# Performance work log

Measured on AMD Instinct MI355X. Metric: run time of the kernel, lower is better.

## Reference

```python
import jax, jax.numpy as jnp
import numpy as np

B, C, D, L, H = 128, 1000, 300, 40, 100


def setup_inputs() -> dict:
    key = jax.random.key(0)
    ks = jax.random.split(key, 16)
    def rn(i, shape, sc=1.0):
        return (jax.random.normal(ks[i], shape, jnp.float32) * sc).astype(jnp.float32)
    return {
        "utt": rn(0, (B, L, D)),
        "sys_slots": rn(1, (B, D), 0.1),
        "conf_slots": rn(2, (B, D), 0.1),
        "conf_values": rn(3, (B, D), 0.1),
        "y_past_state": jax.random.uniform(ks[4], (B, C), jnp.float32),
        "slot_emb": rn(5, (C, D), 0.1),
        "value_emb": rn(6, (C, D), 0.1),
        "Wc": rn(7, (D, 2 * D), 0.05), "bc": jnp.zeros((D,), jnp.float32),
        "conv_w1": rn(8, (D, D, 1), 0.05), "conv_b1": jnp.zeros((D,), jnp.float32),
        "conv_w2": rn(9, (D, D, 2), 0.05), "conv_b2": jnp.zeros((D,), jnp.float32),
        "conv_w3": rn(10, (D, D, 3), 0.05), "conv_b3": jnp.zeros((D,), jnp.float32),
        "Wd": rn(11, (H, D), 0.05), "bd": jnp.zeros((H,), jnp.float32),
        "Wmr": rn(12, (H, D), 0.05), "bmr": jnp.zeros((H,), jnp.float32),
        "Wmc": rn(13, (H, D), 0.05), "bmc": jnp.zeros((H,), jnp.float32),
        "Wj": rn(14, (1, H), 0.05), "bj": jnp.zeros((1,), jnp.float32),
    }


def _conv_relu_pool(x_ncl, w, b):
    # x_ncl: [B, D, L]; w: [F, D, k] -> relu(conv) then global max-pool over time -> [B, F]
    y = jax.lax.conv_general_dilated(x_ncl, w, (1,), 'VALID',
                                     dimension_numbers=('NCH', 'OIH', 'NCH'))
    y = jax.nn.relu(y + b[None, :, None])
    return jnp.max(y, axis=2)


def _sig_linear(x, W, b):
    # Sequential(Sigmoid, Linear): Linear applied to sigmoid(x)
    return jax.nn.sigmoid(x) @ W.T + b


def reference(utt, sys_slots, conf_slots, conf_values, y_past_state,
              slot_emb, value_emb, Wc, bc,
              conv_w1, conv_b1, conv_w2, conv_b2, conv_w3, conv_b3,
              Wd, bd, Wmr, bmr, Wmc, bmc, Wj, bj):
    # CNN utterance encoder: sum of 3 conv branches (filter widths 1,2,3)
    x = jnp.transpose(utt, (0, 2, 1))  # [B, D, L]
    final_utt = (_conv_relu_pool(x, conv_w1, conv_b1)
                 + _conv_relu_pool(x, conv_w2, conv_b2)
                 + _conv_relu_pool(x, conv_w3, conv_b3))  # [B, D]

    # candidates_transform = sigmoid(Linear(cat(slot_emb, value_emb)))
    cand = jax.nn.sigmoid(jnp.concatenate([slot_emb, value_emb], axis=1) @ Wc.T + bc)  # [C, D]

    # fused version of the per-batch repeat/addcmul loop: [B, C, D]
    contrib = cand[None, :, :] * final_utt[:, None, :]

    y1 = _sig_linear(_sig_linear(contrib, Wd, bd), Wj, bj)  # [B, C, 1]

    # system-act request gate: ([C,D]@[D,B]) @ [B,D] -> [C, D]
    m_r = (slot_emb @ sys_slots.T) @ final_utt
    y2 = _sig_linear(_sig_linear(m_r, Wmr, bmr), Wj, bj)  # [C, 1]

    # system-act confirm gate
    m_c = ((slot_emb @ conf_slots.T) * (value_emb @ conf_values.T)) @ final_utt  # [C, D]
    y3 = _sig_linear(_sig_linear(m_c, Wmc, bmc), Wj, bj)  # [C, 1]

    y_presoftmax = y1 + y2[None, :, :] + y3[None, :, :]  # [B, C, 1]
    combine = 0.5
    return combine * y_presoftmax[..., 0] + (1.0 - combine) * y_past_state  # [B, C]
```

## Files before the change

### kernel.cpp

```cpp
#include <hip/hip_runtime.h>
#include <hip/hip_bf16.h>

#define OFF_Y23     0
#define OFF_BDP     4096
#define OFF_WJP     4544
#define OFF_BCP     4992
#define OFF_BMRP    6272
#define OFF_BMCP    6720
#define OFF_WALLT   7168
#define OFF_FUBF    1235968
#define OFF_FUBFT   1317888
#define OFF_CATSV   1399808
#define OFF_WCPK    2710528
#define OFF_CANDBF  3120128
#define OFF_WDFRAG  3775488
#define OFF_WMRFRAG 3847168
#define OFF_WMCFRAG 3918848
#define OFF_SYSB    3990528
#define OFF_CONFSB  4072448
#define OFF_CONFVB  4154368
#define OFF_PRBF    4236288
#define OFF_PCBF    4498432
#define OFF_SMRBF   4760576
#define OFF_SMCBF   5415936
#define OFF_XBF     6071296

typedef short bf16x8_t __attribute__((ext_vector_type(8)));
typedef float f32x4_t  __attribute__((ext_vector_type(4)));

__device__ __forceinline__ float sigmoidf_fast(float x) {
    return __builtin_amdgcn_rcpf(1.0f + __expf(-x));
}
__device__ __forceinline__ unsigned short f2bf(float x) {
    unsigned int u = __float_as_uint(x);
    unsigned int r = (u + 0x7FFFu + ((u >> 16) & 1u)) >> 16;
    return (unsigned short)r;
}
__device__ __forceinline__ float bf2f(unsigned short h) {
    return __uint_as_float(((unsigned int)h) << 16);
}

__global__ __launch_bounds__(256) void pack_kernel(const float* __restrict__ w1,
        const float* __restrict__ w2, const float* __restrict__ w3,
        const float* __restrict__ Wc, const float* __restrict__ Wd,
        const float* __restrict__ Wmr, const float* __restrict__ Wmc,
        const float* __restrict__ sys, const float* __restrict__ confs,
        const float* __restrict__ confv, const float* __restrict__ bd,
        const float* __restrict__ Wj, const float* __restrict__ bmr,
        const float* __restrict__ bmc, const float* __restrict__ bc,
        const float* __restrict__ slot, const float* __restrict__ value,
        const float* __restrict__ utt,
        unsigned short* __restrict__ WallTbf, unsigned short* __restrict__ WdFrag,
        unsigned short* __restrict__ WmrFrag, unsigned short* __restrict__ WmcFrag,
        float* __restrict__ bdPad, float* __restrict__ WjPad,
        float* __restrict__ bmrPad, float* __restrict__ bmcPad,
        float* __restrict__ bcPad,
        unsigned short* __restrict__ sysB, unsigned short* __restrict__ confsB,
        unsigned short* __restrict__ confvB, unsigned short* __restrict__ catsv,
        unsigned short* __restrict__ WcPk, unsigned short* __restrict__ Xbf) {
    int t = blockIdx.x * 256 + threadIdx.x;
    union { unsigned short u[8]; uint4 q; } o;
    if (t < 76800) {
        int i8 = t * 8;
        int tap = i8 / 102400;
        int rem = i8 - tap * 102400;
        int f = rem / 320, k0 = rem % 320;
        #pragma unroll
        for (int e = 0; e < 8; e++) {
            int k = k0 + e;
            float v = 0.0f;
            if (f < 300 && k < 300) {
                int fd = f * 300 + k;
                v = (tap == 0) ? w1[fd] : (tap == 1) ? w2[fd * 2]
                  : (tap == 2) ? w2[fd * 2 + 1] : w3[fd * 3 + (tap - 3)];
            }
            o.u[e] = f2bf(v);
        }
        *(uint4*)(WallTbf + i8) = o.q;
    } else if (t < 90240) {
        int ent = t - 76800;
        int mat = ent / 4480;
        int le = ent - mat * 4480;
        const float* W = (mat == 0) ? Wd : ((mat == 1) ? Wmr : Wmc);
        unsigned short* dst = (mat == 0) ? WdFrag : ((mat == 1) ? WmrFrag : WmcFrag);
        int kt = le / 448;
        int r = le - kt * 448;
        int ni = r >> 6, lane = r & 63;
        int j = ni * 16 + (lane & 15);
        int kb = kt * 32 + (lane >> 4) * 8;
        #pragma unroll
        for (int e = 0; e < 8; e++) {
            int k = kb + e;
            o.u[e] = f2bf((j < 100 && k < 300) ? W[j * 300 + k] : 0.0f);
        }
        *(uint4*)(dst + le * 8) = o.q;
    } else if (t < 105600) {
        int i8 = (t - 90240) * 8;
        int m = i8 / 40960, r = i8 - m * 40960;
        int bb = r / 320, k0 = r % 320;
        const float* src = (m == 0) ? sys : ((m == 1) ? confs : confv);
        unsigned short* dst = (m == 0) ? sysB : ((m == 1) ? confsB : confvB);
        #pragma unroll
        for (int e = 0; e < 8; e++) {
            int k = k0 + e;
            o.u[e] = f2bf((k < 300) ? src[bb * 300 + k] : 0.0f);
        }
        *(uint4*)(dst + r) = o.q;
    } else if (t < 187520) {
        int i8 = (t - 105600) * 8;
        int c = i8 / 640, k0 = i8 % 640;
        #pragma unroll
        for (int e = 0; e < 8; e++) {
            int k = k0 + e;
            float v = 0.0f;
            if (c < 1000) {
                if (k < 300)                  v = slot[c * 300 + k];
                else if (k >= 320 && k < 620) v = value[c * 300 + (k - 320)];
            }
            o.u[e] = f2bf(v);
        }
        *(uint4*)(catsv + i8) = o.q;
    } else if (t < 213120) {
        int i8 = (t - 187520) * 8;
        int f = i8 / 640, k0 = i8 % 640;
        #pragma unroll
        for (int e = 0; e < 8; e++) {
            int k = k0 + e;
            float v = 0.0f;
            if (f < 300) {
                if (k < 300)                  v = Wc[f * 600 + k];
                else if (k >= 320 && k < 620) v = Wc[f * 600 + 300 + (k - 320)];
            }
            o.u[e] = f2bf(v);
        }
        *(uint4*)(WcPk + i8) = o.q;
    } else if (t < 417920) {
        int i8 = (t - 213120) * 8;
        int m = i8 / 320, k0 = i8 % 320;
        if (k0 + 8 <= 300) {
            float4 a = *(const float4*)(utt + m * 300 + k0);
            float4 b = *(const float4*)(utt + m * 300 + k0 + 4);
            o.u[0] = f2bf(a.x); o.u[1] = f2bf(a.y); o.u[2] = f2bf(a.z); o.u[3] = f2bf(a.w);
            o.u[4] = f2bf(b.x); o.u[5] = f2bf(b.y); o.u[6] = f2bf(b.z); o.u[7] = f2bf(b.w);
        } else {
            #pragma unroll
            for (int e = 0; e < 8; e++) {
                int k = k0 + e;
                o.u[e] = f2bf((k < 300) ? utt[m * 300 + k] : 0.0f);
            }
        }
        *(uint4*)(Xbf + i8) = o.q;
    } else if (t < 418688) {
        int j = t - 417920;
        if (j < 112)      bdPad[j] = (j < 100) ? bd[j] : 0.0f;
        else if (j < 224) { int jj = j - 112; WjPad[jj]  = (jj < 100) ? Wj[jj]  : 0.0f; }
        else if (j < 336) { int jj = j - 224; bmrPad[jj] = (jj < 100) ? bmr[jj] : 0.0f; }
        else if (j < 448) { int jj = j - 336; bmcPad[jj] = (jj < 100) ? bmc[jj] : 0.0f; }
        else              { int jj = j - 448; bcPad[jj]  = (jj < 300) ? bc[jj]  : 0.0f; }
    }
}

__global__ __launch_bounds__(256, 4) void early_kernel(
        const unsigned short* __restrict__ Xbf, const unsigned short* __restrict__ WallTbf,
        const float* __restrict__ b1, const float* __restrict__ b2,
        const float* __restrict__ b3,
        unsigned short* __restrict__ fubf, unsigned short* __restrict__ fubfT,
        const unsigned short* __restrict__ catsv, const unsigned short* __restrict__ WcPk,
        const float* __restrict__ bcPad, unsigned short* __restrict__ candbf,
        const unsigned short* __restrict__ sysB, const unsigned short* __restrict__ confsB,
        const unsigned short* __restrict__ confvB,
        unsigned short* __restrict__ Prbf, unsigned short* __restrict__ Pcbf) {
    __shared__ __attribute__((aligned(16))) char smem[25600];
    const int bid = blockIdx.x;
    const int tid = threadIdx.x;
    const int lane = tid & 63, w = tid >> 6;
    const int ln = lane & 15, lq = lane >> 4;

    if (bid >= 112) {
        short* As = (short*)smem;
        short* Bs = (short*)(smem + 3840);
        short* Ps = (short*)smem;
        const int g = bid - 112;
        const int xcd = g & 7;
        const int idx2 = g >> 3;
        const int b = xcd * 16 + idx2 / 10;
        const int fb = idx2 % 10;
        f32x4_t acc[3][3];
        #pragma unroll
        for (int i = 0; i < 3; i++)
            #pragma unroll
            for (int j = 0; j < 3; j++) acc[i][j] = (f32x4_t){0.f, 0.f, 0.f, 0.f};

        const int arow = tid >> 2, aq = tid & 3;
        int agrow = b * 40 + arow; if (agrow > 5119) agrow = 5119;
        const unsigned short* aSrc = Xbf + agrow * 320 + aq * 8;
        const unsigned short* bSrc[3];
        #pragma unroll
        for (int s = 0; s < 3; s++) {
            int i2 = tid + 256 * s;
            int nr = i2 >> 2, q = i2 & 3;
            int tap = nr >> 5, f = fb * 32 + (nr & 31);
            bSrc[s] = WallTbf + (tap * 320 + f) * 320 + q * 8;
        }
        uint4 pa = {0, 0, 0, 0}, pb[3];
        if (tid < 192) pa = *(const uint4*)aSrc;
        #pragma unroll
        for (int s = 0; s < 3; s++) pb[s] = *(const uint4*)bSrc[s];
        if (tid < 192) *(uint4*)(&As[arow * 40 + aq * 8]) = pa;
        #pragma unroll
        for (int s = 0; s < 3; s++) {
            int i2 = tid + 256 * s;
            int nr = i2 >> 2, q = i2 & 3;
            *(uint4*)(&Bs[nr * 40 + q * 8]) = pb[s];
        }
        __syncthreads();

        #pragma unroll 1
        for (int kt = 0; kt < 10; kt++) {
            if (kt < 9) {
                int kk2 = (kt + 1) * 32;
                if (tid < 192) pa = *(const uint4*)(aSrc + kk2);
                #pragma unroll
                for (int s = 0; s < 3; s++) pb[s] = *(const uint4*)(bSrc[s] + kk2);
            }
            bf16x8_t a[3], bb[3];
            #pragma unroll
            for (int mi = 0; mi < 3; mi++)
                a[mi] = *(const bf16x8_t*)(&As[(mi * 16 + ln) * 40 + lq * 8]);
            #pragma unroll
            for (int ni = 0; ni < 3; ni++)
                bb[ni] = *(const bf16x8_t*)(&Bs[(w * 48 + ni * 16 + ln) * 40 + lq * 8]);
            #pragma unroll
            for (int mi = 0; mi < 3; mi++)
                #pragma unroll
                for (int ni = 0; ni < 3; ni++)
                    acc[mi][ni] = __builtin_amdgcn_mfma_f32_16x16x32_bf16(a[mi], bb[ni], acc[mi][ni], 0, 0, 0);
            if (kt < 9) {
                __syncthreads();
                if (tid < 192) *(uint4*)(&As[arow * 40 + aq * 8]) = pa;
                #pragma unroll
                for (int s = 0; s < 3; s++) {
                    int i2 = tid + 256 * s;
                    int nr = i2 >> 2, q = i2 & 3;
                    *(uint4*)(&Bs[nr * 40 + q * 8]) = pb[s];
                }
                __syncthreads();
            }
        }
        __syncthreads();
        #pragma unroll
        for (int mi = 0; mi < 3; mi++)
            #pragma unroll
            for (int ni = 0; ni < 3; ni++)
                #pragma unroll
                for (int reg = 0; reg < 4; reg++)
                    Ps[(mi * 16 + lq * 4 + reg) * 200 + (w * 48 + ni * 16 + ln)] =
                        (short)f2bf(acc[mi][ni][reg]);
        __syncthreads();
        if (tid < 32) {
            int f = fb * 32 + tid;
            if (f < 300) {
                float m1 = -1e30f, m2 = -1e30f, m3 = -1e30f;
                float p1prev = 0.f, p3prev = 0.f, p3prev2 = 0.f, p4prev = 0.f;
                for (int tt = 0; tt < 40; ++tt) {
                    const short* r = Ps + tt * 200;
                    float p0 = bf2f((unsigned short)r[tid]);
                    float p1 = bf2f((unsigned short)r[32 + tid]);
                    float p2 = bf2f((unsigned short)r[64 + tid]);
                    float p3 = bf2f((unsigned short)r[96 + tid]);
                    float p4 = bf2f((unsigned short)r[128 + tid]);
                    float p5 = bf2f((unsigned short)r[160 + tid]);
                    m1 = fmaxf(m1, p0);
                    if (tt >= 1) m2 = fmaxf(m2, p1prev + p2);
                    if (tt >= 2) m3 = fmaxf(m3, p3prev2 + p4prev + p5);
                    p3prev2 = p3prev; p3prev = p3; p4prev = p4; p1prev = p1;
                }
                float r = fmaxf(m1 + b1[f], 0.f) + fmaxf(m2 + b2[f], 0.f)
                        + fmaxf(m3 + b3[f], 0.f);
                unsigned short rb = f2bf(r);
                fubf[b * 320 + f]  = rb;
                fubfT[f * 128 + b] = rb;
            } else {
                fubf[b * 320 + f]  = 0;
                fubfT[f * 128 + b] = 0;
            }
        }
    } else if (bid < 80) {
        short* As = (short*)smem;
        short* Bs = (short*)(smem + 5120);
        const int m0 = (bid / 5) * 64, n0 = (bid % 5) * 64;
        const int wr = w & 1, wc = w >> 1;
        f32x4_t acc[2][2];
        #pragma unroll
        for (int i = 0; i < 2; i++)
            #pragma unroll
            for (int j = 0; j < 2; j++) acc[i][j] = (f32x4_t){0.f, 0.f, 0.f, 0.f};
        const int srow = tid >> 2, sq = tid & 3;
        for (int kk = 0; kk < 640; kk += 32) {
            *(uint4*)(&As[srow * 40 + sq * 8]) = *(const uint4*)(catsv + (m0 + srow) * 640 + kk + sq * 8);
            *(uint4*)(&Bs[srow * 40 + sq * 8]) = *(const uint4*)(WcPk  + (n0 + srow) * 640 + kk + sq * 8);
            __syncthreads();
            bf16x8_t a[2], b[2];
            #pragma unroll
            for (int mi = 0; mi < 2; mi++)
                a[mi] = *(const bf16x8_t*)(&As[(wr * 32 + mi * 16 + ln) * 40 + lq * 8]);
            #pragma unroll
            for (int ni = 0; ni < 2; ni++)
                b[ni] = *(const bf16x8_t*)(&Bs[(wc * 32 + ni * 16 + ln) * 40 + lq * 8]);
            #pragma unroll
            for (int mi = 0; mi < 2; mi++)
                #pragma unroll
                for (int ni = 0; ni < 2; ni++)
                    acc[mi][ni] = __builtin_amdgcn_mfma_f32_16x16x32_bf16(a[mi], b[ni], acc[mi][ni], 0, 0, 0);
            __syncthreads();
        }
        #pragma unroll
        for (int mi = 0; mi < 2; mi++) {
            #pragma unroll
            for (int ni = 0; ni < 2; ni++) {
                int n = n0 + wc * 32 + ni * 16 + ln;
                float bcv = bcPad[n];
                #pragma unroll
                for (int reg = 0; reg < 4; reg++) {
                    int cr = m0 + wr * 32 + mi * 16 + lq * 4 + reg;
                    candbf[cr * 320 + n] = f2bf(sigmoidf_fast(acc[mi][ni][reg] + bcv));
                }
            }
        }
    } else {
        short* As0 = (short*)smem;
        short* As1 = (short*)(smem + 5120);
        short* Bs0 = (short*)(smem + 10240);
        short* Bs1 = (short*)(smem + 15360);
        short* Bs2 = (short*)(smem + 20480);
        const int pid = bid - 80;
        const int c0 = (pid >> 1) * 64;
        const int bh = (pid & 1) * 64;
        f32x4_t accR[4], accS[4], accV[4];
        #pragma unroll
        for (int i = 0; i < 4; i++) {
            accR[i] = (f32x4_t){0.f, 0.f, 0.f, 0.f};
            accS[i] = (f32x4_t){0.f, 0.f, 0.f, 0.f};
            accV[i] = (f32x4_t){0.f, 0.f, 0.f, 0.f};
        }
        for (int kk = 0; kk < 320; kk += 32) {
            #pragma unroll
            for (int i = tid; i < 512; i += 256) {
                int mat = i >> 8, r2 = i & 255;
                int row = r2 >> 2, q = r2 & 3;
                short* dst = mat ? As1 : As0;
                *(uint4*)(&dst[row * 40 + q * 8]) =
                    *(const uint4*)(catsv + (c0 + row) * 640 + mat * 320 + kk + q * 8);
            }
            #pragma unroll
            for (int i = tid; i < 768; i += 256) {
                int mat = i >> 8, r2 = i & 255;
                int row = r2 >> 2, q = r2 & 3;
                const unsigned short* src = (mat == 0) ? sysB : ((mat == 1) ? confsB : confvB);
                short* dst = (mat == 0) ? Bs0 : ((mat == 1) ? Bs1 : Bs2);
                *(uint4*)(&dst[row * 40 + q * 8]) =
                    *(const uint4*)(src + (bh + row) * 320 + kk + q * 8);
            }
            __syncthreads();
            bf16x8_t aS = *(const bf16x8_t*)(&As0[(w * 16 + ln) * 40 + lq * 8]);
            bf16x8_t aV = *(const bf16x8_t*)(&As1[(w * 16 + ln) * 40 + lq * 8]);
            #pragma unroll
            for (int ni = 0; ni < 4; ni++) {
                bf16x8_t bR = *(const bf16x8_t*)(&Bs0[(ni * 16 + ln) * 40 + lq * 8]);
                bf16x8_t bS = *(const bf16x8_t*)(&Bs1[(ni * 16 + ln) * 40 + lq * 8]);
                bf16x8_t bV = *(const bf16x8_t*)(&Bs2[(ni * 16 + ln) * 40 + lq * 8]);
                accR[ni] = __builtin_amdgcn_mfma_f32_16x16x32_bf16(aS, bR, accR[ni], 0, 0, 0);
                accS[ni] = __builtin_amdgcn_mfma_f32_16x16x32_bf16(aS, bS, accS[ni], 0, 0, 0);
                accV[ni] = __builtin_amdgcn_mfma_f32_16x16x32_bf16(aV, bV, accV[ni], 0, 0, 0);
            }
            __syncthreads();
        }
        #pragma unroll
        for (int ni = 0; ni < 4; ni++) {
            int b = bh + ni * 16 + ln;
            #pragma unroll
            for (int reg = 0; reg < 4; reg++) {
                int c = c0 + w * 16 + lq * 4 + reg;
                Prbf[c * 128 + b] = f2bf(accR[ni][reg]);
                Pcbf[c * 128 + b] = f2bf(accS[ni][reg] * accV[ni][reg]);
            }
        }
    }
}

__global__ __launch_bounds__(256) void mgate_gemm(const unsigned short* __restrict__ Prbf,
        const unsigned short* __restrict__ Pcbf, const unsigned short* __restrict__ fubfT,
        unsigned short* __restrict__ smrbf, unsigned short* __restrict__ smcbf) {
    __shared__ __attribute__((aligned(16))) short As[2][64 * 40];
    __shared__ __attribute__((aligned(16))) short Bs[64 * 40];
    const int tid = threadIdx.x;
    const int m0 = blockIdx.x * 64, n0 = blockIdx.y * 64;
    const int lane = tid & 63, w = tid >> 6;
    const int wr = w & 1, wc = w >> 1;
    const int ln = lane & 15, lq = lane >> 4;
    f32x4_t accR[2][2], accC[2][2];
    #pragma unroll
    for (int i = 0; i < 2; i++)
        #pragma unroll
        for (int j = 0; j < 2; j++) {
            accR[i][j] = (f32x4_t){0.f, 0.f, 0.f, 0.f};
            accC[i][j] = (f32x4_t){0.f, 0.f, 0.f, 0.f};
        }
    for (int kk = 0; kk < 128; kk += 32) {
        #pragma unroll
        for (int i = tid; i < 512; i += 256) {
            int mat = i >> 8, r2 = i & 255;
            int row = r2 >> 2, q = r2 & 3;
            const unsigned short* src = mat ? Pcbf : Prbf;
            *(uint4*)(&As[mat][row * 40 + q * 8]) =
                *(const uint4*)(src + (m0 + row) * 128 + kk + q * 8);
        }
        if (tid < 256) {
            int row = tid >> 2, q = tid & 3;
            *(uint4*)(&Bs[row * 40 + q * 8]) =
                *(const uint4*)(fubfT + (n0 + row) * 128 + kk + q * 8);
        }
        __syncthreads();
        bf16x8_t aR[2], aC[2], b[2];
        #pragma unroll
        for (int mi = 0; mi < 2; mi++) {
            aR[mi] = *(const bf16x8_t*)(&As[0][(wr * 32 + mi * 16 + ln) * 40 + lq * 8]);
            aC[mi] = *(const bf16x8_t*)(&As[1][(wr * 32 + mi * 16 + ln) * 40 + lq * 8]);
        }
        #pragma unroll
        for (int ni = 0; ni < 2; ni++)
            b[ni] = *(const bf16x8_t*)(&Bs[(wc * 32 + ni * 16 + ln) * 40 + lq * 8]);
        #pragma unroll
        for (int mi = 0; mi < 2; mi++)
            #pragma unroll
            for (int ni = 0; ni < 2; ni++) {
                accR[mi][ni] = __builtin_amdgcn_mfma_f32_16x16x32_bf16(aR[mi], b[ni], accR[mi][ni], 0, 0, 0);
                accC[mi][ni] = __builtin_amdgcn_mfma_f32_16x16x32_bf16(aC[mi], b[ni], accC[mi][ni], 0, 0, 0);
            }
        __syncthreads();
    }
    #pragma unroll
    for (int mi = 0; mi < 2; mi++) {
        #pragma unroll
        for (int ni = 0; ni < 2; ni++) {
            int f = n0 + wc * 32 + ni * 16 + ln;
            #pragma unroll
            for (int reg = 0; reg < 4; reg++) {
                int c = m0 + wr * 32 + mi * 16 + lq * 4 + reg;
                smrbf[c * 320 + f] = f2bf(sigmoidf_fast(accR[mi][ni][reg]));
                smcbf[c * 320 + f] = f2bf(sigmoidf_fast(accC[mi][ni][reg]));
            }
        }
    }
}

__global__ __launch_bounds__(256) void ygate_gemm(const unsigned short* __restrict__ smrbf,
        const unsigned short* __restrict__ smcbf, const unsigned short* __restrict__ WmrFrag,
        const unsigned short* __restrict__ WmcFrag, const float* __restrict__ bmrPad,
        const float* __restrict__ bmcPad, const float* __restrict__ WjPad,
        const float* __restrict__ bj, float* __restrict__ y23) {
    __shared__ __attribute__((aligned(16))) short As[2][64 * 40];
    __shared__ __attribute__((aligned(16))) short Bs[2][3584];
    const int tid = threadIdx.x;
    const int c0 = blockIdx.x * 64;
    const int lane = tid & 63, w = tid >> 6;
    const int ln = lane & 15, lq = lane >> 4;
    f32x4_t accR[7], accC[7];
    #pragma unroll
    for (int i = 0; i < 7; i++) {
        accR[i] = (f32x4_t){0.f, 0.f, 0.f, 0.f};
        accC[i] = (f32x4_t){0.f, 0.f, 0.f, 0.f};
    }
    for (int kt = 0; kt < 10; kt++) {
        int kk = kt * 32;
        #pragma unroll
        for (int i = tid; i < 512; i += 256) {
            int mat = i >> 8, r2 = i & 255;
            int row = r2 >> 2, q = r2 & 3;
            const unsigned short* src = mat ? smcbf : smrbf;
            *(uint4*)(&As[mat][row * 40 + q * 8]) =
                *(const uint4*)(src + (c0 + row) * 320 + kk + q * 8);
        }
        #pragma unroll
        for (int i = tid; i < 896; i += 256) {
            int mat = i / 448, j = i - mat * 448;
            const uint4* s = (const uint4*)((mat ? WmcFrag : WmrFrag) + kt * 3584);
            ((uint4*)&Bs[mat][0])[j] = s[j];
        }
        __syncthreads();
        bf16x8_t aR = *(const bf16x8_t*)(&As[0][(w * 16 + ln) * 40 + lq * 8]);
        bf16x8_t aC = *(const bf16x8_t*)(&As[1][(w * 16 + ln) * 40 + lq * 8]);
        #pragma unroll
        for (int ni = 0; ni < 7; ni++) {
            bf16x8_t bR = *(const bf16x8_t*)(&Bs[0][(ni * 64 + lane) * 8]);
            bf16x8_t bC = *(const bf16x8_t*)(&Bs[1][(ni * 64 + lane) * 8]);
            accR[ni] = __builtin_amdgcn_mfma_f32_16x16x32_bf16(aR, bR, accR[ni], 0, 0, 0);
            accC[ni] = __builtin_amdgcn_mfma_f32_16x16x32_bf16(aC, bC, accC[ni], 0, 0, 0);
        }
        __syncthreads();
    }
    float psum[4] = {0.f, 0.f, 0.f, 0.f};
    #pragma unroll
    for (int ni = 0; ni < 7; ni++) {
        int n = ni * 16 + ln;
        float wj = WjPad[n], br = bmrPad[n], bcv = bmcPad[n];
        #pragma unroll
        for (int reg = 0; reg < 4; reg++) {
            float hr = sigmoidf_fast(accR[ni][reg] + br);
            float hc = sigmoidf_fast(accC[ni][reg] + bcv);
            psum[reg] += (hr + hc) * wj;
        }
    }
    #pragma unroll
    for (int reg = 0; reg < 4; reg++) {
        float v = psum[reg];
        v += __shfl_xor(v, 1);
        v += __shfl_xor(v, 2);
        v += __shfl_xor(v, 4);
        v += __shfl_xor(v, 8);
        if (ln == 0) {
            int c = c0 + w * 16 + lq * 4 + reg;
            y23[c] = v + 2.0f * bj[0];
        }
    }
}

__global__ __launch_bounds__(256) void gemm2_kernel(const unsigned short* __restrict__ candbf,
        const unsigned short* __restrict__ fubf, const unsigned short* __restrict__ WdFrag,
        const float* __restrict__ bdPad, const float* __restrict__ WjPad,
        const float* __restrict__ bj, const float* __restrict__ y23,
        const float* __restrict__ ypast, float* __restrict__ out) {
    __shared__ __attribute__((aligned(16))) short Bs[2][3584];
    __shared__ float bdS[112], WjS[112], ybuf[128];
    const int c = blockIdx.x;
    const int tid = threadIdx.x;
    const int lane = tid & 63, w = tid >> 6;
    const int ln = lane & 15, lq = lane >> 4;
    if (tid < 112) { bdS[tid] = bdPad[tid]; WjS[tid] = WjPad[tid]; }

    const unsigned short* candRow = candbf + c * 320;
    const unsigned short* fuR0 = fubf + (w * 32 + ln) * 320;
    const unsigned short* fuR1 = fuR0 + 16 * 320;

    f32x4_t acc[2][7];
    #pragma unroll
    for (int mi = 0; mi < 2; mi++)
        #pragma unroll
        for (int ni = 0; ni < 7; ni++) acc[mi][ni] = (f32x4_t){0.f, 0.f, 0.f, 0.f};

    {
        const uint4* src = (const uint4*)(WdFrag);
        uint4* dst = (uint4*)&Bs[0][0];
        dst[tid] = src[tid];
        if (tid < 192) dst[tid + 256] = src[tid + 256];
    }
    __syncthreads();

    #pragma unroll
    for (int kt = 0; kt < 10; kt++) {
        if (kt < 9) {
            const uint4* src = (const uint4*)(WdFrag + (kt + 1) * 3584);
            uint4* dst = (uint4*)&Bs[(kt + 1) & 1][0];
            dst[tid] = src[tid];
            if (tid < 192) dst[tid + 256] = src[tid + 256];
        }
        const int k0 = kt * 32 + lq * 8;
        bf16x8_t cf  = *(const bf16x8_t*)(candRow + k0);
        bf16x8_t f0v = *(const bf16x8_t*)(fuR0 + k0);
        bf16x8_t f1v = *(const bf16x8_t*)(fuR1 + k0);
        bf16x8_t a0, a1;
        #pragma unroll
        for (int e = 0; e < 8; e += 2) {
            float cv0 = bf2f((unsigned short)cf[e]);
            float cv1 = bf2f((unsigned short)cf[e + 1]);
            float2 s0 = make_float2(sigmoidf_fast(cv0 * bf2f((unsigned short)f0v[e])),
                                    sigmoidf_fast(cv1 * bf2f((unsigned short)f0v[e + 1])));
            float2 s1 = make_float2(sigmoidf_fast(cv0 * bf2f((unsigned short)f1v[e])),
                                    sigmoidf_fast(cv1 * bf2f((unsigned short)f1v[e + 1])));
            __hip_bfloat162 p0 = __float22bfloat162_rn(s0);
            __hip_bfloat162 p1 = __float22bfloat162_rn(s1);
            ((unsigned int*)&a0)[e >> 1] = *(unsigned int*)&p0;
            ((unsigned int*)&a1)[e >> 1] = *(unsigned int*)&p1;
        }
        #pragma unroll
        for (int ni = 0; ni < 7; ni++) {
            bf16x8_t bfr = *(const bf16x8_t*)(&Bs[kt & 1][(ni * 64 + lane) * 8]);
            acc[0][ni] = __builtin_amdgcn_mfma_f32_16x16x32_bf16(a0, bfr, acc[0][ni], 0, 0, 0);
            acc[1][ni] = __builtin_amdgcn_mfma_f32_16x16x32_bf16(a1, bfr, acc[1][ni], 0, 0, 0);
        }
        __syncthreads();
    }

    float psum[2][4] = {{0.f, 0.f, 0.f, 0.f}, {0.f, 0.f, 0.f, 0.f}};
    #pragma unroll
    for (int mi = 0; mi < 2; mi++) {
        #pragma unroll
        for (int ni = 0; ni < 7; ni++) {
            int n = ni * 16 + ln;
            float bdv = bdS[n], wjv = WjS[n];
            #pragma unroll
            for (int reg = 0; reg < 4; reg++) {
                float h = sigmoidf_fast(acc[mi][ni][reg] + bdv);
                psum[mi][reg] += h * wjv;
            }
        }
    }
    #pragma unroll
    for (int mi = 0; mi < 2; mi++) {
        #pragma unroll
        for (int reg = 0; reg < 4; reg++) {
            float v = psum[mi][reg];
            v += __shfl_xor(v, 1);
            v += __shfl_xor(v, 2);
            v += __shfl_xor(v, 4);
            v += __shfl_xor(v, 8);
            if (ln == 0) ybuf[w * 32 + mi * 16 + lq * 4 + reg] = v;
        }
    }
    __syncthreads();
    if (tid < 128) {
        int b = tid;
        float y1 = ybuf[b] + bj[0];
        out[b * 1000 + c] = 0.5f * (y1 + y23[c]) + 0.5f * ypast[b * 1000 + c];
    }
}

extern "C" void kernel_launch(void* const* d_in, const int* in_sizes, int n_in,
                              void* d_out, int out_size, void* d_ws, size_t ws_size,
                              hipStream_t stream) {
    const float* utt   = (const float*)d_in[0];
    const float* sys   = (const float*)d_in[1];
    const float* confs = (const float*)d_in[2];
    const float* confv = (const float*)d_in[3];
    const float* ypast = (const float*)d_in[4];
    const float* slot  = (const float*)d_in[5];
    const float* value = (const float*)d_in[6];
    const float* Wc    = (const float*)d_in[7];
    const float* bc    = (const float*)d_in[8];
    const float* w1    = (const float*)d_in[9];
    const float* b1    = (const float*)d_in[10];
    const float* w2    = (const float*)d_in[11];
    const float* b2    = (const float*)d_in[12];
    const float* w3    = (const float*)d_in[13];
    const float* b3    = (const float*)d_in[14];
    const float* Wd    = (const float*)d_in[15];
    const float* bd    = (const float*)d_in[16];
    const float* Wmr   = (const float*)d_in[17];
    const float* bmr   = (const float*)d_in[18];
    const float* Wmc   = (const float*)d_in[19];
    const float* bmc   = (const float*)d_in[20];
    const float* Wj    = (const float*)d_in[21];
    const float* bj    = (const float*)d_in[22];

    char* wsb = (char*)d_ws;
    float* y23    = (float*)(wsb + OFF_Y23);
    float* bdPad  = (float*)(wsb + OFF_BDP);
    float* WjPad  = (float*)(wsb + OFF_WJP);
    float* bcPad  = (float*)(wsb + OFF_BCP);
    float* bmrPad = (float*)(wsb + OFF_BMRP);
    float* bmcPad = (float*)(wsb + OFF_BMCP);
    unsigned short* WallTbf = (unsigned short*)(wsb + OFF_WALLT);
    unsigned short* fubf    = (unsigned short*)(wsb + OFF_FUBF);
    unsigned short* fubfT   = (unsigned short*)(wsb + OFF_FUBFT);
    unsigned short* catsv   = (unsigned short*)(wsb + OFF_CATSV);
    unsigned short* WcPk    = (unsigned short*)(wsb + OFF_WCPK);
    unsigned short* candbf  = (unsigned short*)(wsb + OFF_CANDBF);
    unsigned short* WdFrag  = (unsigned short*)(wsb + OFF_WDFRAG);
    unsigned short* WmrFrag = (unsigned short*)(wsb + OFF_WMRFRAG);
    unsigned short* WmcFrag = (unsigned short*)(wsb + OFF_WMCFRAG);
    unsigned short* sysB    = (unsigned short*)(wsb + OFF_SYSB);
    unsigned short* confsB  = (unsigned short*)(wsb + OFF_CONFSB);
    unsigned short* confvB  = (unsigned short*)(wsb + OFF_CONFVB);
    unsigned short* Prbf    = (unsigned short*)(wsb + OFF_PRBF);
    unsigned short* Pcbf    = (unsigned short*)(wsb + OFF_PCBF);
    unsigned short* smrbf   = (unsigned short*)(wsb + OFF_SMRBF);
    unsigned short* smcbf   = (unsigned short*)(wsb + OFF_SMCBF);
    unsigned short* Xbf     = (unsigned short*)(wsb + OFF_XBF);
    float* out = (float*)d_out;

    pack_kernel<<<1636, 256, 0, stream>>>(w1, w2, w3, Wc, Wd, Wmr, Wmc, sys, confs, confv,
                                          bd, Wj, bmr, bmc, bc, slot, value, utt,
                                          WallTbf, WdFrag, WmrFrag, WmcFrag,
                                          bdPad, WjPad, bmrPad, bmcPad, bcPad,
                                          sysB, confsB, confvB, catsv, WcPk, Xbf);
    early_kernel<<<1392, 256, 0, stream>>>(Xbf, WallTbf, b1, b2, b3, fubf, fubfT,
                                           catsv, WcPk, bcPad, candbf,
                                           sysB, confsB, confvB, Prbf, Pcbf);
    mgate_gemm<<<dim3(16, 5), 256, 0, stream>>>(Prbf, Pcbf, fubfT, smrbf, smcbf);
    ygate_gemm<<<16, 256, 0, stream>>>(smrbf, smcbf, WmrFrag, WmcFrag,
                                       bmrPad, bmcPad, WjPad, bj, y23);
    gemm2_kernel<<<1000, 256, 0, stream>>>(candbf, fubf, WdFrag, bdPad, WjPad,
                                           bj, y23, ypast, out);
}
```

Before: 214.5 us.

## Split conv GEMM from max-pool into plain tiled GEMM plus combine kernel

The conv branch of early_kernel changes from per-batch, per-filter-block tiles that did the max-pool in shared memory to a plain 64x128 GEMM tile over all 5120 rows and 1920 tap columns. The full bf16 pre-activation matrix is written to a new ~19.6MB workspace buffer. A new combine_kernel then does the shifted-sum, max-pool, bias and ReLU. This drops the wasted rows of the 48-row padding and the serial 32-thread epilogue, but adds a large global write/read round trip and one more launch.

```diff
diff --git a/kernel.cpp b/kernel.cpp
--- a/kernel.cpp
+++ b/kernel.cpp
@@ -8,22 +8,23 @@
 #define OFF_BMRP    6272
 #define OFF_BMCP    6720
 #define OFF_WALLT   7168
-#define OFF_FUBF    1235968
-#define OFF_FUBFT   1317888
-#define OFF_CATSV   1399808
-#define OFF_WCPK    2710528
-#define OFF_CANDBF  3120128
-#define OFF_WDFRAG  3775488
-#define OFF_WMRFRAG 3847168
-#define OFF_WMCFRAG 3918848
-#define OFF_SYSB    3990528
-#define OFF_CONFSB  4072448
-#define OFF_CONFVB  4154368
-#define OFF_PRBF    4236288
-#define OFF_PCBF    4498432
-#define OFF_SMRBF   4760576
-#define OFF_SMCBF   5415936
-#define OFF_XBF     6071296
+#define OFF_PBF     1235968
+#define OFF_FUBF    20896768
+#define OFF_FUBFT   20978688
+#define OFF_CATSV   21060608
+#define OFF_WCPK    22371328
+#define OFF_CANDBF  22780928
+#define OFF_WDFRAG  23436288
+#define OFF_WMRFRAG 23507968
+#define OFF_WMCFRAG 23579648
+#define OFF_SYSB    23651328
+#define OFF_CONFSB  23733248
+#define OFF_CONFVB  23815168
+#define OFF_PRBF    23897088
+#define OFF_PCBF    24159232
+#define OFF_SMRBF   24421376
+#define OFF_SMCBF   25076736
+#define OFF_XBF     25732096
 
 typedef short bf16x8_t __attribute__((ext_vector_type(8)));
 typedef float f32x4_t  __attribute__((ext_vector_type(4)));
@@ -162,9 +163,7 @@
 
 __global__ __launch_bounds__(256, 4) void early_kernel(
         const unsigned short* __restrict__ Xbf, const unsigned short* __restrict__ WallTbf,
-        const float* __restrict__ b1, const float* __restrict__ b2,
-        const float* __restrict__ b3,
-        unsigned short* __restrict__ fubf, unsigned short* __restrict__ fubfT,
+        unsigned short* __restrict__ Pbf,
         const unsigned short* __restrict__ catsv, const unsigned short* __restrict__ WcPk,
         const float* __restrict__ bcPad, unsigned short* __restrict__ candbf,
         const unsigned short* __restrict__ sysB, const unsigned short* __restrict__ confsB,
@@ -178,111 +177,68 @@
 
     if (bid >= 112) {
         short* As = (short*)smem;
-        short* Bs = (short*)(smem + 3840);
-        short* Ps = (short*)smem;
+        short* Bs = (short*)(smem + 5120);
         const int g = bid - 112;
         const int xcd = g & 7;
         const int idx2 = g >> 3;
-        const int b = xcd * 16 + idx2 / 10;
-        const int fb = idx2 % 10;
-        f32x4_t acc[3][3];
-        #pragma unroll
-        for (int i = 0; i < 3; i++)
-            #pragma unroll
-            for (int j = 0; j < 3; j++) acc[i][j] = (f32x4_t){0.f, 0.f, 0.f, 0.f};
-
+        const int m0 = (xcd * 10 + idx2 / 15) * 64;
+        const int n0 = (idx2 % 15) * 128;
         const int arow = tid >> 2, aq = tid & 3;
-        int agrow = b * 40 + arow; if (agrow > 5119) agrow = 5119;
-        const unsigned short* aSrc = Xbf + agrow * 320 + aq * 8;
-        const unsigned short* bSrc[3];
-        #pragma unroll
-        for (int s = 0; s < 3; s++) {
-            int i2 = tid + 256 * s;
-            int nr = i2 >> 2, q = i2 & 3;
-            int tap = nr >> 5, f = fb * 32 + (nr & 31);
-            bSrc[s] = WallTbf + (tap * 320 + f) * 320 + q * 8;
-        }
-        uint4 pa = {0, 0, 0, 0}, pb[3];
-        if (tid < 192) pa = *(const uint4*)aSrc;
-        #pragma unroll
-        for (int s = 0; s < 3; s++) pb[s] = *(const uint4*)bSrc[s];
-        if (tid < 192) *(uint4*)(&As[arow * 40 + aq * 8]) = pa;
-        #pragma unroll
-        for (int s = 0; s < 3; s++) {
-            int i2 = tid + 256 * s;
-            int nr = i2 >> 2, q = i2 & 3;
-            *(uint4*)(&Bs[nr * 40 + q * 8]) = pb[s];
-        }
+        f32x4_t acc[4][2];
+        #pragma unroll
+        for (int i = 0; i < 4; i++)
+            #pragma unroll
+            for (int j = 0; j < 2; j++) acc[i][j] = (f32x4_t){0.f, 0.f, 0.f, 0.f};
+
+        const unsigned short* aSrc  = Xbf + (m0 + arow) * 320 + aq * 8;
+        const unsigned short* bSrc0 = WallTbf + (n0 + arow) * 320 + aq * 8;
+        const unsigned short* bSrc1 = WallTbf + (n0 + 64 + arow) * 320 + aq * 8;
+        uint4 pa  = *(const uint4*)(aSrc);
+        uint4 pb0 = *(const uint4*)(bSrc0);
+        uint4 pb1 = *(const uint4*)(bSrc1);
+        *(uint4*)(&As[arow * 40 + aq * 8]) = pa;
+        *(uint4*)(&Bs[arow * 40 + aq * 8]) = pb0;
+        *(uint4*)(&Bs[(64 + arow) * 40 + aq * 8]) = pb1;
         __syncthreads();
 
         #pragma unroll 1
         for (int kt = 0; kt < 10; kt++) {
             if (kt < 9) {
                 int kk2 = (kt + 1) * 32;
-                if (tid < 192) pa = *(const uint4*)(aSrc + kk2);
+                pa  = *(const uint4*)(aSrc + kk2);
+                pb0 = *(const uint4*)(bSrc0 + kk2);
+                pb1 = *(const uint4*)(bSrc1 + kk2);
+            }
+            bf16x8_t a[4], b[2];
+            #pragma unroll
+            for (int mi = 0; mi < 4; mi++)
+                a[mi] = *(const bf16x8_t*)(&As[(mi * 16 + ln) * 40 + lq * 8]);
+            #pragma unroll
+            for (int ni = 0; ni < 2; ni++)
+                b[ni] = *(const bf16x8_t*)(&Bs[(w * 32 + ni * 16 + ln) * 40 + lq * 8]);
+            #pragma unroll
+            for (int mi = 0; mi < 4; mi++)
                 #pragma unroll
-                for (int s = 0; s < 3; s++) pb[s] = *(const uint4*)(bSrc[s] + kk2);
-            }
-            bf16x8_t a[3], bb[3];
-            #pragma unroll
-            for (int mi = 0; mi < 3; mi++)
-                a[mi] = *(const bf16x8_t*)(&As[(mi * 16 + ln) * 40 + lq * 8]);
-            #pragma unroll
-            for (int ni = 0; ni < 3; ni++)
-                bb[ni] = *(const bf16x8_t*)(&Bs[(w * 48 + ni * 16 + ln) * 40 + lq * 8]);
-            #pragma unroll
-            for (int mi = 0; mi < 3; mi++)
-                #pragma unroll
-                for (int ni = 0; ni < 3; ni++)
-                    acc[mi][ni] = __builtin_amdgcn_mfma_f32_16x16x32_bf16(a[mi], bb[ni], acc[mi][ni], 0, 0, 0);
+                for (int ni = 0; ni < 2; ni++)
+                    acc[mi][ni] = __builtin_amdgcn_mfma_f32_16x16x32_bf16(a[mi], b[ni], acc[mi][ni], 0, 0, 0);
             if (kt < 9) {
                 __syncthreads();
-                if (tid < 192) *(uint4*)(&As[arow * 40 + aq * 8]) = pa;
+                *(uint4*)(&As[arow * 40 + aq * 8]) = pa;
+                *(uint4*)(&Bs[arow * 40 + aq * 8]) = pb0;
+                *(uint4*)(&Bs[(64 + arow) * 40 + aq * 8]) = pb1;
+                __syncthreads();
+            }
+        }
+        #pragma unroll
+        for (int mi = 0; mi < 4; mi++) {
+            #pragma unroll
+            for (int ni = 0; ni < 2; ni++) {
+                int col = n0 + w * 32 + ni * 16 + ln;
                 #pragma unroll
-                for (int s = 0; s < 3; s++) {
-                    int i2 = tid + 256 * s;
-                    int nr = i2 >> 2, q = i2 & 3;
-                    *(uint4*)(&Bs[nr * 40 + q * 8]) = pb[s];
+                for (int reg = 0; reg < 4; reg++) {
+                    int row = m0 + mi * 16 + lq * 4 + reg;
+                    Pbf[row * 1920 + col] = f2bf(acc[mi][ni][reg]);
                 }
-                __syncthreads();
-            }
-        }
-        __syncthreads();
-        #pragma unroll
-        for (int mi = 0; mi < 3; mi++)
-            #pragma unroll
-            for (int ni = 0; ni < 3; ni++)
-                #pragma unroll
-                for (int reg = 0; reg < 4; reg++)
-                    Ps[(mi * 16 + lq * 4 + reg) * 200 + (w * 48 + ni * 16 + ln)] =
-                        (short)f2bf(acc[mi][ni][reg]);
-        __syncthreads();
-        if (tid < 32) {
-            int f = fb * 32 + tid;
-            if (f < 300) {
-                float m1 = -1e30f, m2 = -1e30f, m3 = -1e30f;
-                float p1prev = 0.f, p3prev = 0.f, p3prev2 = 0.f, p4prev = 0.f;
-                for (int tt = 0; tt < 40; ++tt) {
-                    const short* r = Ps + tt * 200;
-                    float p0 = bf2f((unsigned short)r[tid]);
-                    float p1 = bf2f((unsigned short)r[32 + tid]);
-                    float p2 = bf2f((unsigned short)r[64 + tid]);
-                    float p3 = bf2f((unsigned short)r[96 + tid]);
-                    float p4 = bf2f((unsigned short)r[128 + tid]);
-                    float p5 = bf2f((unsigned short)r[160 + tid]);
-                    m1 = fmaxf(m1, p0);
-                    if (tt >= 1) m2 = fmaxf(m2, p1prev + p2);
-                    if (tt >= 2) m3 = fmaxf(m3, p3prev2 + p4prev + p5);
-                    p3prev2 = p3prev; p3prev = p3; p4prev = p4; p1prev = p1;
-                }
-                float r = fmaxf(m1 + b1[f], 0.f) + fmaxf(m2 + b2[f], 0.f)
-                        + fmaxf(m3 + b3[f], 0.f);
-                unsigned short rb = f2bf(r);
-                fubf[b * 320 + f]  = rb;
-                fubfT[f * 128 + b] = rb;
-            } else {
-                fubf[b * 320 + f]  = 0;
-                fubfT[f * 128 + b] = 0;
             }
         }
     } else if (bid < 80) {
@@ -386,6 +342,35 @@
             }
         }
     }
+}
+
+__global__ __launch_bounds__(64) void combine_kernel(const unsigned short* __restrict__ Pbf,
+        const float* __restrict__ b1, const float* __restrict__ b2,
+        const float* __restrict__ b3, unsigned short* __restrict__ fubf,
+        unsigned short* __restrict__ fubfT) {
+    int b = blockIdx.x;
+    int f = blockIdx.y * 64 + threadIdx.x;
+    if (f >= 300) { fubf[b * 320 + f] = 0; fubfT[f * 128 + b] = 0; return; }
+    const unsigned short* base = Pbf + (size_t)b * 40 * 1920;
+    float m1 = -1e30f, m2 = -1e30f, m3 = -1e30f;
+    float p1prev = 0.f, p3prev = 0.f, p3prev2 = 0.f, p4prev = 0.f;
+    for (int t = 0; t < 40; ++t) {
+        const unsigned short* r = base + t * 1920;
+        float p0 = bf2f(r[f]);
+        float p1 = bf2f(r[320 + f]);
+        float p2 = bf2f(r[640 + f]);
+        float p3 = bf2f(r[960 + f]);
+        float p4 = bf2f(r[1280 + f]);
+        float p5 = bf2f(r[1600 + f]);
+        m1 = fmaxf(m1, p0);
+        if (t >= 1) m2 = fmaxf(m2, p1prev + p2);
+        if (t >= 2) m3 = fmaxf(m3, p3prev2 + p4prev + p5);
+        p3prev2 = p3prev; p3prev = p3; p4prev = p4; p1prev = p1;
+    }
+    float r = fmaxf(m1 + b1[f], 0.f) + fmaxf(m2 + b2[f], 0.f) + fmaxf(m3 + b3[f], 0.f);
+    unsigned short rb = f2bf(r);
+    fubf[b * 320 + f]  = rb;
+    fubfT[f * 128 + b] = rb;
 }
 
 __global__ __launch_bounds__(256) void mgate_gemm(const unsigned short* __restrict__ Prbf,
@@ -660,6 +645,7 @@
     float* bmrPad = (float*)(wsb + OFF_BMRP);
     float* bmcPad = (float*)(wsb + OFF_BMCP);
     unsigned short* WallTbf = (unsigned short*)(wsb + OFF_WALLT);
+    unsigned short* Pbf     = (unsigned short*)(wsb + OFF_PBF);
     unsigned short* fubf    = (unsigned short*)(wsb + OFF_FUBF);
     unsigned short* fubfT   = (unsigned short*)(wsb + OFF_FUBFT);
     unsigned short* catsv   = (unsigned short*)(wsb + OFF_CATSV);
@@ -683,9 +669,10 @@
                                           WallTbf, WdFrag, WmrFrag, WmcFrag,
                                           bdPad, WjPad, bmrPad, bmcPad, bcPad,
                                           sysB, confsB, confvB, catsv, WcPk, Xbf);
-    early_kernel<<<1392, 256, 0, stream>>>(Xbf, WallTbf, b1, b2, b3, fubf, fubfT,
+    early_kernel<<<1312, 256, 0, stream>>>(Xbf, WallTbf, Pbf,
                                            catsv, WcPk, bcPad, candbf,
                                            sysB, confsB, confvB, Prbf, Pcbf);
+    combine_kernel<<<dim3(128, 5), 64, 0, stream>>>(Pbf, b1, b2, b3, fubf, fubfT);
     mgate_gemm<<<dim3(16, 5), 256, 0, stream>>>(Prbf, Pcbf, fubfT, smrbf, smcbf);
     ygate_gemm<<<16, 256, 0, stream>>>(smrbf, smcbf, WmrFrag, WmcFrag,
                                        bmrPad, bmcPad, WjPad, bj, y23);
```

New measurement: 191.5 us, median of 2. 10.7% less time.
